# Kernel optimization log

Measured on AMD Instinct MI355X. Metric: run time of the kernel, lower is better.

## Reference

```python
import jax, jax.numpy as jnp
import numpy as np

B, D, H, L = 4096, 8192, 4096, 128


def binarize_ste(v, thresh):
    # BinarizeTensorThresh with straight-through gradient (identity backward)
    return v + jax.lax.stop_gradient((v > thresh).astype(v.dtype) - v)


def setup_inputs() -> dict:
    key = jax.random.key(0)
    k0, k1, k2, k3 = jax.random.split(key, 4)
    x = (jax.random.uniform(k0, (B, D), jnp.float32) < 0.1).astype(jnp.float32)  # sparse binary data
    enc_weight = jax.random.normal(k1, (H, D), jnp.float32) * (2.0 / (H + D)) ** 0.5 + 0.5  # xavier-ish around binarize thresh
    bias0 = -jax.random.uniform(k2, (H,), jnp.float32)  # clipBias keeps bias <= 0
    bias3 = jnp.zeros((D,), jnp.float32)  # act3.noBias()
    clf_weight = jax.random.uniform(k3, (L, H), jnp.float32)  # clamped to [0,1]
    return {"x": x, "enc_weight": enc_weight, "bias0": bias0, "bias3": bias3, "clf_weight": clf_weight}


def reference(x, enc_weight, bias0, bias3, clf_weight):
    wb = binarize_ste(enc_weight, 0.5)                 # [H, D] binarized encoder weights
    h = jnp.einsum('bd,hd->bh', x, wb)                 # fc0_enc
    z = binarize_ste(h + bias0, 1.0)                   # act0: BinaryActivation (STE threshold)
    classification = jnp.einsum('bh,lh->bl', z, clf_weight)  # classifier (no bias)
    recon = jnp.einsum('bh,hd->bd', z, wb)             # fc3_dec: tied transposed binarized weights
    output = binarize_ste(recon + bias3, 1.0)          # act3
    return output, classification, z
```

## Files before the change

### kernel.cpp

```cpp
#include <hip/hip_runtime.h>
#include <cstdint>

typedef unsigned long long u64;

constexpr int B = 4096;
constexpr int D = 8192;
constexpr int H = 4096;
constexpr int L = 128;
constexpr int DW = D / 64;
constexpr int HW = H / 64;

__global__ __launch_bounds__(256) void k_P(const float* __restrict__ e,
                                           u64* __restrict__ wbpw) {
    __shared__ u64 sw[DW];
    unsigned char* sb = (unsigned char*)sw;
    int h = blockIdx.x;
    const float4* row4 = (const float4*)(e + (size_t)h * D);
    #pragma unroll
    for (int j = 0; j < 4; ++j) {
        int t = j * 256 + threadIdx.x;
        float4 a = row4[2 * t];
        float4 c = row4[2 * t + 1];
        unsigned v = (a.x > 0.5f ? 1u : 0u) | (a.y > 0.5f ? 2u : 0u)
                   | (a.z > 0.5f ? 4u : 0u) | (a.w > 0.5f ? 8u : 0u)
                   | (c.x > 0.5f ? 16u : 0u) | (c.y > 0.5f ? 32u : 0u)
                   | (c.z > 0.5f ? 64u : 0u) | (c.w > 0.5f ? 128u : 0u);
        sb[t] = (unsigned char)v;
    }
    __syncthreads();
    if (threadIdx.x < DW)
        wbpw[(size_t)threadIdx.x * H + h] = sw[threadIdx.x];
}

__global__ __launch_bounds__(256) void k_B(const u64* __restrict__ wbpw,
                                           const float* __restrict__ bias0,
                                           const float* __restrict__ bias3,
                                           const float* __restrict__ clf,
                                           float* __restrict__ basef,
                                           int* __restrict__ cmin,
                                           float* __restrict__ R) {
    __shared__ int sc[4][64];
    __shared__ float s[256];
    int r = blockIdx.x;
    int lane = threadIdx.x & 63;
    int wave = threadIdx.x >> 6;
    if (r < DW) {
        int w = r;
        int cnt = 0;
        #pragma unroll 1
        for (int g = wave; g < 64; g += 4) {
            u64 W = wbpw[(size_t)w * H + g * 64 + lane];
            #pragma unroll 1
            for (int jj = 0; jj < 64; ++jj) {
                u64 m = __ballot((int)((W >> jj) & 1ull));
                if (lane == jj) cnt += (int)__popcll(m);
            }
        }
        sc[wave][lane] = cnt;
        __syncthreads();
        if (wave == 0) {
            int tot = sc[0][lane] + sc[1][lane] + sc[2][lane] + sc[3][lane];
            int d = w * 64 + lane;
            basef[d] = ((float)tot + bias3[d] > 1.0f) ? 1.0f : 0.0f;
        }
    } else if (r < DW + 16) {
        int h = (r - DW) * 256 + threadIdx.x;
        float b0 = bias0[h];
        int c = (int)(1.0f - b0);
        if (c < 0) c = 0;
        int guard = 0;
        while ((float)c + b0 <= 1.0f && guard++ < 100000) ++c;
        while (c > 0 && (float)(c - 1) + b0 > 1.0f) --c;
        cmin[h] = c;
    } else {
        int l = r - (DW + 16);
        float acc = 0.f;
        for (int hh = threadIdx.x; hh < H; hh += 256) acc += clf[(size_t)l * H + hh];
        s[threadIdx.x] = acc;
        __syncthreads();
        for (int off = 128; off > 0; off >>= 1) {
            if ((int)threadIdx.x < off) s[threadIdx.x] += s[threadIdx.x + off];
            __syncthreads();
        }
        if (threadIdx.x == 0) R[l] = s[0];
    }
}

__global__ __launch_bounds__(256) void k_Z(const float* __restrict__ x,
                                           const u64* __restrict__ wbpw,
                                           const int* __restrict__ cmin,
                                           const float* __restrict__ basef,
                                           const float* __restrict__ R,
                                           const float* __restrict__ clf,
                                           const float* __restrict__ bias3,
                                           float* __restrict__ out0,
                                           float* __restrict__ out1,
                                           float* __restrict__ zout) {
    __shared__ u64 sxw[DW];
    __shared__ u64 zrow[HW];
    __shared__ int s_nz;
    unsigned char* sxb = (unsigned char*)sxw;
    int b = blockIdx.x;
    int lane = threadIdx.x & 63;
    int wave = threadIdx.x >> 6;

    const float4* xr4 = (const float4*)(x + (size_t)b * D);
    #pragma unroll
    for (int j = 0; j < 4; ++j) {
        int t = j * 256 + threadIdx.x;
        float4 a = xr4[2 * t];
        float4 c = xr4[2 * t + 1];
        unsigned v = (a.x > 0.5f ? 1u : 0u) | (a.y > 0.5f ? 2u : 0u)
                   | (a.z > 0.5f ? 4u : 0u) | (a.w > 0.5f ? 8u : 0u)
                   | (c.x > 0.5f ? 16u : 0u) | (c.y > 0.5f ? 32u : 0u)
                   | (c.z > 0.5f ? 64u : 0u) | (c.w > 0.5f ? 128u : 0u);
        sxb[t] = (unsigned char)v;
    }
    __syncthreads();
    u64 x0 = sxw[0], x1 = sxw[1], x2 = sxw[2], x3 = sxw[3];

    #pragma unroll 1
    for (int i = 0; i < HW / 4; ++i) {
        int hb = wave * (HW / 4) + i;
        int h = hb * 64 + lane;
        int cm = cmin[h];
        const u64* __restrict__ wp = wbpw + hb * 64 + lane;
        u64 w0 = wp[0];
        u64 w1 = wp[(size_t)H];
        u64 w2 = wp[(size_t)2 * H];
        u64 w3 = wp[(size_t)3 * H];
        int cnt = (int)__popcll(x0 & w0) + (int)__popcll(x1 & w1)
                + (int)__popcll(x2 & w2) + (int)__popcll(x3 & w3);
        if (!__all(cnt >= cm)) {
            #pragma unroll 1
            for (int w = 4; w < DW; ++w) {
                if (cnt < cm) cnt += (int)__popcll(sxw[w] & wp[(size_t)w * H]);
                if (__all(cnt >= cm)) break;
            }
        }
        int zb = (cnt >= cm) ? 1 : 0;
        u64 m = __ballot(zb);
        if (lane == 0) zrow[hb] = m;
    }
    __syncthreads();

    if (wave == 0) {
        int c = (int)__popcll(zrow[lane]);
        #pragma unroll
        for (int off = 32; off > 0; off >>= 1) c += __shfl_down(c, off);
        if (lane == 0) s_nz = H - c;
    }
    __syncthreads();
    int nz = s_nz;

    {
        float* zr = zout + (size_t)b * H;
        #pragma unroll
        for (int k = 0; k < 4; ++k) {
            int t = threadIdx.x + k * 256;
            u64 wzd = zrow[t >> 4];
            int j0 = (t & 15) * 4;
            float4 f;
            f.x = ((wzd >> (j0 + 0)) & 1ull) ? 1.0f : 0.0f;
            f.y = ((wzd >> (j0 + 1)) & 1ull) ? 1.0f : 0.0f;
            f.z = ((wzd >> (j0 + 2)) & 1ull) ? 1.0f : 0.0f;
            f.w = ((wzd >> (j0 + 3)) & 1ull) ? 1.0f : 0.0f;
            ((float4*)zr)[t] = f;
        }
    }

    if (nz == 0) {
        if (threadIdx.x < L) out1[(size_t)b * L + threadIdx.x] = R[threadIdx.x];
        float4* o4 = (float4*)(out0 + (size_t)b * D);
        const float4* b4 = (const float4*)basef;
        #pragma unroll
        for (int k = 0; k < 8; ++k) {
            int t = threadIdx.x + k * 256;
            o4[t] = b4[t];
        }
    } else {
        if (threadIdx.x < L) {
            int l = threadIdx.x;
            float acc = 0.f;
            for (int wh = 0; wh < HW; ++wh) {
                u64 m = zrow[wh];
                while (m) {
                    int j = __ffsll(m) - 1;
                    acc += clf[(size_t)l * H + wh * 64 + j];
                    m &= m - 1;
                }
            }
            out1[(size_t)b * L + l] = acc;
        }
        for (int w = wave; w < DW; w += 4) {
            int acc = 0;
            for (int hb = 0; hb < HW; ++hb) {
                u64 Wj = wbpw[(size_t)w * H + hb * 64 + lane];
                u64 zm = zrow[hb];
                u64 masked = ((zm >> lane) & 1ull) ? Wj : 0ull;
                for (int jj = 0; jj < 64; ++jj) {
                    u64 bal = __ballot((int)((masked >> jj) & 1ull));
                    if (lane == jj) acc += (int)__popcll(bal);
                }
            }
            int d = w * 64 + lane;
            out0[(size_t)b * D + d] = ((float)acc + bias3[d] > 1.0f) ? 1.0f : 0.0f;
        }
    }
}


extern "C" void kernel_launch(void* const* d_in, const int* in_sizes, int n_in,
                              void* d_out, int out_size, void* d_ws, size_t ws_size,
                              hipStream_t stream) {
    const float* x   = (const float*)d_in[0];
    const float* ew  = (const float*)d_in[1];
    const float* b0  = (const float*)d_in[2];
    const float* b3  = (const float*)d_in[3];
    const float* clf = (const float*)d_in[4];

    float* out0 = (float*)d_out;
    float* out1 = out0 + (size_t)B * D;
    float* zout = out1 + (size_t)B * L;

    char* ws = (char*)d_ws;
    u64* wbpw    = (u64*)(ws);
    float* basef = (float*)(ws + (4ull << 20));
    float* R     = (float*)(ws + (4ull << 20) + 32768);
    int* cmin    = (int*)(ws + (4ull << 20) + 32768 + 512);

    k_P<<<H, 256, 0, stream>>>(ew, wbpw);
    k_B<<<DW + 16 + L, 256, 0, stream>>>(wbpw, b0, b3, clf, basef, cmin, R);
    k_Z<<<B, 256, 0, stream>>>(x, wbpw, cmin, basef, R, clf, b3,
                               out0, out1, zout);
}
```

Baseline: 454.9 us.

## Process four batch rows per block and binarize x lazily

The Z kernel now handles four batch rows per block. Each wave ballots only the first 256 x values of its row into shared memory, and further x columns are read on demand only when the early popcount cannot decide the activation. This avoids reading and packing every full x row and reuses the weight-word loads across four rows. Encoder weight loads and output stores use nontemporal hints. The cost is fewer blocks and a more serialized fallback path that rereads x from global memory.

```diff
diff --git a/kernel.cpp b/kernel.cpp
--- a/kernel.cpp
+++ b/kernel.cpp
@@ -2,6 +2,7 @@
 #include <cstdint>
 
 typedef unsigned long long u64;
+typedef float f4 __attribute__((ext_vector_type(4)));
 
 constexpr int B = 4096;
 constexpr int D = 8192;
@@ -9,18 +10,19 @@
 constexpr int L = 128;
 constexpr int DW = D / 64;
 constexpr int HW = H / 64;
+constexpr int RB = 4;
 
 __global__ __launch_bounds__(256) void k_P(const float* __restrict__ e,
                                            u64* __restrict__ wbpw) {
     __shared__ u64 sw[DW];
     unsigned char* sb = (unsigned char*)sw;
     int h = blockIdx.x;
-    const float4* row4 = (const float4*)(e + (size_t)h * D);
+    const f4* row4 = (const f4*)(e + (size_t)h * D);
     #pragma unroll
     for (int j = 0; j < 4; ++j) {
         int t = j * 256 + threadIdx.x;
-        float4 a = row4[2 * t];
-        float4 c = row4[2 * t + 1];
+        f4 a = __builtin_nontemporal_load(row4 + 2 * t);
+        f4 c = __builtin_nontemporal_load(row4 + 2 * t + 1);
         unsigned v = (a.x > 0.5f ? 1u : 0u) | (a.y > 0.5f ? 2u : 0u)
                    | (a.z > 0.5f ? 4u : 0u) | (a.w > 0.5f ? 8u : 0u)
                    | (c.x > 0.5f ? 16u : 0u) | (c.y > 0.5f ? 32u : 0u)
@@ -96,28 +98,28 @@
                                            float* __restrict__ out0,
                                            float* __restrict__ out1,
                                            float* __restrict__ zout) {
-    __shared__ u64 sxw[DW];
-    __shared__ u64 zrow[HW];
-    __shared__ int s_nz;
-    unsigned char* sxb = (unsigned char*)sxw;
-    int b = blockIdx.x;
+    __shared__ u64 sxw4[RB][4];
+    __shared__ u64 zrow[RB][HW];
+    __shared__ int s_nz[RB];
+    int b0 = blockIdx.x * RB;
     int lane = threadIdx.x & 63;
     int wave = threadIdx.x >> 6;
 
-    const float4* xr4 = (const float4*)(x + (size_t)b * D);
+    {
+        const float* xr = x + (size_t)(b0 + wave) * D;
+        #pragma unroll
+        for (int j = 0; j < 4; ++j) {
+            u64 m = __ballot(xr[j * 64 + lane] > 0.5f);
+            if (lane == 0) sxw4[wave][j] = m;
+        }
+    }
+    __syncthreads();
+    u64 xa0[RB], xa1[RB], xa2[RB], xa3[RB];
     #pragma unroll
-    for (int j = 0; j < 4; ++j) {
-        int t = j * 256 + threadIdx.x;
-        float4 a = xr4[2 * t];
-        float4 c = xr4[2 * t + 1];
-        unsigned v = (a.x > 0.5f ? 1u : 0u) | (a.y > 0.5f ? 2u : 0u)
-                   | (a.z > 0.5f ? 4u : 0u) | (a.w > 0.5f ? 8u : 0u)
-                   | (c.x > 0.5f ? 16u : 0u) | (c.y > 0.5f ? 32u : 0u)
-                   | (c.z > 0.5f ? 64u : 0u) | (c.w > 0.5f ? 128u : 0u);
-        sxb[t] = (unsigned char)v;
-    }
-    __syncthreads();
-    u64 x0 = sxw[0], x1 = sxw[1], x2 = sxw[2], x3 = sxw[3];
+    for (int r = 0; r < RB; ++r) {
+        xa0[r] = sxw4[r][0]; xa1[r] = sxw4[r][1];
+        xa2[r] = sxw4[r][2]; xa3[r] = sxw4[r][3];
+    }
 
     #pragma unroll 1
     for (int i = 0; i < HW / 4; ++i) {
@@ -129,82 +131,92 @@
         u64 w1 = wp[(size_t)H];
         u64 w2 = wp[(size_t)2 * H];
         u64 w3 = wp[(size_t)3 * H];
-        int cnt = (int)__popcll(x0 & w0) + (int)__popcll(x1 & w1)
-                + (int)__popcll(x2 & w2) + (int)__popcll(x3 & w3);
-        if (!__all(cnt >= cm)) {
-            #pragma unroll 1
-            for (int w = 4; w < DW; ++w) {
-                if (cnt < cm) cnt += (int)__popcll(sxw[w] & wp[(size_t)w * H]);
-                if (__all(cnt >= cm)) break;
-            }
-        }
-        int zb = (cnt >= cm) ? 1 : 0;
-        u64 m = __ballot(zb);
-        if (lane == 0) zrow[hb] = m;
-    }
-    __syncthreads();
-
-    if (wave == 0) {
-        int c = (int)__popcll(zrow[lane]);
+        #pragma unroll
+        for (int r = 0; r < RB; ++r) {
+            int cnt = (int)__popcll(xa0[r] & w0) + (int)__popcll(xa1[r] & w1)
+                    + (int)__popcll(xa2[r] & w2) + (int)__popcll(xa3[r] & w3);
+            if (!__all(cnt >= cm)) {
+                const float* xr = x + (size_t)(b0 + r) * D;
+                #pragma unroll 1
+                for (int w = 4; w < DW; ++w) {
+                    u64 xm = __ballot(xr[w * 64 + lane] > 0.5f);
+                    if (cnt < cm) cnt += (int)__popcll(xm & wp[(size_t)w * H]);
+                    if (__all(cnt >= cm)) break;
+                }
+            }
+            u64 m = __ballot(cnt >= cm);
+            if (lane == 0) zrow[r][hb] = m;
+        }
+    }
+    __syncthreads();
+
+    {
+        int c = (int)__popcll(zrow[wave][lane]);
         #pragma unroll
         for (int off = 32; off > 0; off >>= 1) c += __shfl_down(c, off);
-        if (lane == 0) s_nz = H - c;
-    }
-    __syncthreads();
-    int nz = s_nz;
-
-    {
-        float* zr = zout + (size_t)b * H;
+        if (lane == 0) s_nz[wave] = H - c;
+    }
+    __syncthreads();
+
+    #pragma unroll 1
+    for (int r = 0; r < RB; ++r) {
+        f4* zr = (f4*)(zout + (size_t)(b0 + r) * H);
         #pragma unroll
         for (int k = 0; k < 4; ++k) {
             int t = threadIdx.x + k * 256;
-            u64 wzd = zrow[t >> 4];
+            u64 wzd = zrow[r][t >> 4];
             int j0 = (t & 15) * 4;
-            float4 f;
+            f4 f;
             f.x = ((wzd >> (j0 + 0)) & 1ull) ? 1.0f : 0.0f;
             f.y = ((wzd >> (j0 + 1)) & 1ull) ? 1.0f : 0.0f;
             f.z = ((wzd >> (j0 + 2)) & 1ull) ? 1.0f : 0.0f;
             f.w = ((wzd >> (j0 + 3)) & 1ull) ? 1.0f : 0.0f;
-            ((float4*)zr)[t] = f;
-        }
-    }
-
-    if (nz == 0) {
-        if (threadIdx.x < L) out1[(size_t)b * L + threadIdx.x] = R[threadIdx.x];
-        float4* o4 = (float4*)(out0 + (size_t)b * D);
-        const float4* b4 = (const float4*)basef;
-        #pragma unroll
-        for (int k = 0; k < 8; ++k) {
-            int t = threadIdx.x + k * 256;
-            o4[t] = b4[t];
-        }
-    } else {
-        if (threadIdx.x < L) {
-            int l = threadIdx.x;
-            float acc = 0.f;
-            for (int wh = 0; wh < HW; ++wh) {
-                u64 m = zrow[wh];
-                while (m) {
-                    int j = __ffsll(m) - 1;
-                    acc += clf[(size_t)l * H + wh * 64 + j];
-                    m &= m - 1;
+            __builtin_nontemporal_store(f, zr + t);
+        }
+    }
+
+    #pragma unroll 1
+    for (int r = 0; r < RB; ++r) {
+        int nz = s_nz[r];
+        size_t bb = (size_t)(b0 + r);
+        if (nz == 0) {
+            if (threadIdx.x < L)
+                __builtin_nontemporal_store(R[threadIdx.x], out1 + bb * L + threadIdx.x);
+            f4* o4 = (f4*)(out0 + bb * D);
+            const f4* b4 = (const f4*)basef;
+            #pragma unroll
+            for (int k = 0; k < 8; ++k) {
+                int t = threadIdx.x + k * 256;
+                __builtin_nontemporal_store(b4[t], o4 + t);
+            }
+        } else {
+            if (threadIdx.x < L) {
+                int l = threadIdx.x;
+                float acc = 0.f;
+                for (int wh = 0; wh < HW; ++wh) {
+                    u64 m = zrow[r][wh];
+                    while (m) {
+                        int j = __ffsll(m) - 1;
+                        acc += clf[(size_t)l * H + wh * 64 + j];
+                        m &= m - 1;
+                    }
                 }
-            }
-            out1[(size_t)b * L + l] = acc;
-        }
-        for (int w = wave; w < DW; w += 4) {
-            int acc = 0;
-            for (int hb = 0; hb < HW; ++hb) {
-                u64 Wj = wbpw[(size_t)w * H + hb * 64 + lane];
-                u64 zm = zrow[hb];
-                u64 masked = ((zm >> lane) & 1ull) ? Wj : 0ull;
-                for (int jj = 0; jj < 64; ++jj) {
-                    u64 bal = __ballot((int)((masked >> jj) & 1ull));
-                    if (lane == jj) acc += (int)__popcll(bal);
+                out1[bb * L + l] = acc;
+            }
+            for (int w = wave; w < DW; w += 4) {
+                int acc = 0;
+                for (int hb = 0; hb < HW; ++hb) {
+                    u64 Wj = wbpw[(size_t)w * H + hb * 64 + lane];
+                    u64 zm = zrow[r][hb];
+                    u64 masked = ((zm >> lane) & 1ull) ? Wj : 0ull;
+                    for (int jj = 0; jj < 64; ++jj) {
+                        u64 bal = __ballot((int)((masked >> jj) & 1ull));
+                        if (lane == jj) acc += (int)__popcll(bal);
+                    }
                 }
-            }
-            int d = w * 64 + lane;
-            out0[(size_t)b * D + d] = ((float)acc + bias3[d] > 1.0f) ? 1.0f : 0.0f;
+                int d = w * 64 + lane;
+                out0[bb * D + d] = ((float)acc + bias3[d] > 1.0f) ? 1.0f : 0.0f;
+            }
         }
     }
 }
@@ -231,6 +243,6 @@
 
     k_P<<<H, 256, 0, stream>>>(ew, wbpw);
     k_B<<<DW + 16 + L, 256, 0, stream>>>(wbpw, b0, b3, clf, basef, cmin, R);
-    k_Z<<<B, 256, 0, stream>>>(x, wbpw, cmin, basef, R, clf, b3,
-                               out0, out1, zout);
-}
+    k_Z<<<B / RB, 256, 0, stream>>>(x, wbpw, cmin, basef, R, clf, b3,
+                                    out0, out1, zout);
+}
```

Result: faster. 416.9 us (-8.3%).
